# Kernel optimization log

Measured on AMD Instinct MI355X. Metric: run time of the kernel, lower is better.

The kernel has to match this reference:

```python
import jax, jax.numpy as jnp
import numpy as np

TEMPERATURE = 0.1  # init arg `temperature`


def _l2_normalize(x):
    return x / jnp.sqrt(jnp.sum(x * x, axis=1, keepdims=True))


def setup_inputs() -> dict:
    key = jax.random.key(0)
    k1, k2, k3 = jax.random.split(key, 3)
    B, D, Q = 2048, 128, 65536
    projections_1 = jax.random.normal(k1, (B, D), dtype=jnp.float32)
    projections_2 = jax.random.normal(k2, (B, D), dtype=jnp.float32)
    # queue is initialized row-l2-normalized in the original module
    feature_queue = _l2_normalize(jax.random.normal(k3, (Q, D), dtype=jnp.float32))
    return {"projections_1": projections_1, "projections_2": projections_2,
            "feature_queue": feature_queue}


def reference(projections_1, projections_2, feature_queue):
    # NNCLR.contrastive_loss (per-sample losses), including nearest_neighbour.
    p1 = _l2_normalize(projections_1)  # [B, D]
    p2 = _l2_normalize(projections_2)  # [B, D]

    def nearest_neighbour(p):
        # [B, Q] similarity -> top-1 index -> gather from queue
        sims = jnp.einsum('bd,qd->bq', p, feature_queue)
        idx = jnp.argmax(sims, axis=1)  # [B]
        nn = feature_queue[idx]         # [B, D]
        # straight-through: value = nn, gradient flows to p
        return p + jax.lax.stop_gradient(nn - p)

    nn1 = nearest_neighbour(p1)
    nn2 = nearest_neighbour(p2)

    s_1_2_1 = jnp.einsum('id,jd->ij', nn1, p2) / TEMPERATURE
    s_1_2_2 = jnp.einsum('id,jd->ij', p2, nn1) / TEMPERATURE
    s_2_1_1 = jnp.einsum('id,jd->ij', nn2, p1) / TEMPERATURE
    s_2_1_2 = jnp.einsum('id,jd->ij', p1, nn2) / TEMPERATURE

    logits = jnp.concatenate([s_1_2_1, s_1_2_2, s_2_1_1, s_2_1_2], axis=0)  # [4B, B]
    B = p1.shape[0]
    labels = jnp.tile(jnp.arange(B), 4)  # [4B]
    logp = jax.nn.log_softmax(logits, axis=1)
    loss = -jnp.take_along_axis(logp, labels[:, None], axis=1)[:, 0]  # [4B]
    return loss
```

## Files before the change

### kernel.cpp

```cpp
#include <hip/hip_runtime.h>

#define S 132
#define SCALE 10.0f
#define EPS_MARGIN 0.008f
#define SROWS_CAP 480
#define ROWCHUNK 48
#define STRIP_CAND 256

typedef __attribute__((ext_vector_type(8))) short short8;
typedef __attribute__((ext_vector_type(4))) float floatx4;

#define MFMA16(a, b, c) __builtin_amdgcn_mfma_f32_16x16x32_bf16((a), (b), (c), 0, 0, 0)

__device__ __forceinline__ unsigned int ordered_bits(float f) {
    unsigned int b = __float_as_uint(f);
    return (b & 0x80000000u) ? ~b : (b | 0x80000000u);
}
__device__ __forceinline__ float from_ordered(unsigned int u) {
    return __uint_as_float((u & 0x80000000u) ? (u ^ 0x80000000u) : ~u);
}
__device__ __forceinline__ short bf_rne(float x) {
    unsigned int u = __float_as_uint(x);
    return (short)((u + 0x7FFFu + ((u >> 16) & 1u)) >> 16);
}
__device__ __forceinline__ float bf2f(short s) {
    return __uint_as_float(((unsigned int)(unsigned short)s) << 16);
}

__global__ void k_prep(const float* __restrict__ p1, const float* __restrict__ p2,
                       float* __restrict__ pn, short* __restrict__ pnb,
                       unsigned int* __restrict__ mbest,
                       unsigned long long* __restrict__ best,
                       unsigned int* __restrict__ scnt,
                       float* __restrict__ sums) {
    int row = blockIdx.x;
    int t = threadIdx.x;
    const float* src = (row < 2048) ? (p1 + (size_t)row * 128)
                                    : (p2 + (size_t)(row - 2048) * 128);
    float2 v = ((const float2*)src)[t];
    float ss = v.x * v.x + v.y * v.y;
    #pragma unroll
    for (int o = 32; o; o >>= 1) ss += __shfl_xor(ss, o);
    float inv = 1.0f / sqrtf(ss);
    float2 o2; o2.x = v.x * inv; o2.y = v.y * inv;
    ((float2*)(pn + (size_t)row * 128))[t] = o2;
    unsigned int pk = (unsigned int)(unsigned short)bf_rne(o2.x)
                    | ((unsigned int)(unsigned short)bf_rne(o2.y) << 16);
    ((unsigned int*)(pnb + (size_t)row * 128))[t] = pk;
    if (t == 0) { mbest[row] = 0u; best[row] = 0ULL; if (row < 1024) scnt[row] = 0u; }
    if (row < 128) sums[row * 64 + t] = 0.0f;
}

__global__ void k_qcvt(const float* __restrict__ queue, short* __restrict__ qb) {
    size_t i = ((size_t)blockIdx.x * 256 + threadIdx.x) * 8;
    float4 f0 = *(const float4*)(queue + i);
    float4 f1 = *(const float4*)(queue + i + 4);
    short8 o;
    o[0] = bf_rne(f0.x); o[1] = bf_rne(f0.y); o[2] = bf_rne(f0.z); o[3] = bf_rne(f0.w);
    o[4] = bf_rne(f1.x); o[5] = bf_rne(f1.y); o[6] = bf_rne(f1.z); o[7] = bf_rne(f1.w);
    *(short8*)(qb + i) = o;
}

__device__ __forceinline__ void screen_tile(const short8 A[8][4],
                                            short8 b0, short8 b1, short8 b2, short8 b3,
                                            float rmax[8][4]) {
    floatx4 acc[8];
    floatx4 zero = {0.0f, 0.0f, 0.0f, 0.0f};
    #pragma unroll
    for (int rf = 0; rf < 8; ++rf) acc[rf] = MFMA16(A[rf][0], b0, zero);
    #pragma unroll
    for (int rf = 0; rf < 8; ++rf) acc[rf] = MFMA16(A[rf][1], b1, acc[rf]);
    #pragma unroll
    for (int rf = 0; rf < 8; ++rf) acc[rf] = MFMA16(A[rf][2], b2, acc[rf]);
    #pragma unroll
    for (int rf = 0; rf < 8; ++rf) acc[rf] = MFMA16(A[rf][3], b3, acc[rf]);
    #pragma unroll
    for (int rf = 0; rf < 8; ++rf)
        #pragma unroll
        for (int r = 0; r < 4; ++r) rmax[rf][r] = fmaxf(rmax[rf][r], acc[rf][r]);
}

__global__ __launch_bounds__(256, 2) void k_screen(const short* __restrict__ pnb,
                                                   const short* __restrict__ qb,
                                                   unsigned int* __restrict__ mbest,
                                                   float* __restrict__ smax) {
    int tid = threadIdx.x;
    int lane = tid & 63, wv = tid >> 6;
    int n16 = lane & 15, quad = lane >> 4;

    int id = blockIdx.x;
    int xcd = id & 7;
    int g = id >> 3;
    int rowblk = g & 7;
    int qsub = g >> 3;
    int qsplit = xcd * 8 + qsub;
    int rowbase = rowblk * 512 + wv * 128;
    int qstart = qsplit * 1024;

    short8 A[8][4];
    #pragma unroll
    for (int rf = 0; rf < 8; ++rf) {
        const short* ap = pnb + (size_t)(rowbase + rf * 16 + n16) * 128 + quad * 8;
        #pragma unroll
        for (int kk = 0; kk < 4; ++kk)
            A[rf][kk] = *(const short8*)(ap + kk * 32);
    }
    #pragma unroll
    for (int rf = 0; rf < 8; ++rf)
        #pragma unroll
        for (int kk = 0; kk < 4; ++kk)
            asm volatile("" : "+v"(A[rf][kk]));

    float rmax[8][4];
    #pragma unroll
    for (int rf = 0; rf < 8; ++rf)
        #pragma unroll
        for (int r = 0; r < 4; ++r) rmax[rf][r] = -1e30f;

    const short* lp = qb + (size_t)(qstart + n16) * 128 + quad * 8;
    short8 a0 = *(const short8*)(lp), a1 = *(const short8*)(lp + 32),
           a2 = *(const short8*)(lp + 64), a3 = *(const short8*)(lp + 96);

    for (int t = 0; t < 64; t += 2) {
        if ((t & 15) == 0) __syncthreads();
        const short* p1p = lp + 2048;
        short8 b0 = *(const short8*)(p1p), b1 = *(const short8*)(p1p + 32),
               b2 = *(const short8*)(p1p + 64), b3 = *(const short8*)(p1p + 96);
        screen_tile(A, a0, a1, a2, a3, rmax);
        const short* p2p = lp + 4096;
        a0 = *(const short8*)(p2p); a1 = *(const short8*)(p2p + 32);
        a2 = *(const short8*)(p2p + 64); a3 = *(const short8*)(p2p + 96);
        screen_tile(A, b0, b1, b2, b3, rmax);
        lp += 4096;
    }

    #pragma unroll
    for (int rf = 0; rf < 8; ++rf)
        #pragma unroll
        for (int r = 0; r < 4; ++r) {
            float v = rmax[rf][r];
            v = fmaxf(v, __shfl_xor(v, 1));
            v = fmaxf(v, __shfl_xor(v, 2));
            v = fmaxf(v, __shfl_xor(v, 4));
            v = fmaxf(v, __shfl_xor(v, 8));
            if (n16 == 0) {
                int row = rowbase + rf * 16 + quad * 4 + r;
                atomicMax(&mbest[row], ordered_bits(v));
                smax[(size_t)qsplit * 4096 + row] = v;
            }
        }
}

__global__ __launch_bounds__(256) void k_rows(const unsigned int* __restrict__ mbest,
                                              const float* __restrict__ smax,
                                              int* __restrict__ rcnt,
                                              unsigned short* __restrict__ rlist) {
    __shared__ unsigned short rows[SROWS_CAP];
    __shared__ int nsh;
    int tid = threadIdx.x;
    int s = blockIdx.x;
    if (tid == 0) nsh = 0;
    __syncthreads();
    const float* sm = smax + (size_t)s * 4096;
    #pragma unroll
    for (int j = 0; j < 16; ++j) {
        int row = tid + 256 * j;
        float thr = from_ordered(mbest[row]) - EPS_MARGIN;
        if (sm[row] > thr) {
            int pos = atomicAdd(&nsh, 1);
            if (pos < SROWS_CAP) rows[pos] = (unsigned short)row;
        }
    }
    __syncthreads();
    int n = nsh; if (n > SROWS_CAP) n = SROWS_CAP;
    if (tid == 0) rcnt[s] = n;
    for (int i = tid; i < n; i += 256) rlist[s * SROWS_CAP + i] = rows[i];
}

__global__ __launch_bounds__(256, 4) void k_rescreen(const short* __restrict__ pnb,
                                                     const short* __restrict__ qb,
                                                     const unsigned int* __restrict__ mbest,
                                                     const int* __restrict__ rcnt,
                                                     const unsigned short* __restrict__ rlist,
                                                     unsigned int* __restrict__ scnt,
                                                     unsigned int* __restrict__ cand) {
    int b = blockIdx.x;
    int s = b & 63;
    int qp = b >> 6;
    int n = rcnt[s];
    if (n == 0) return;

    int tid = threadIdx.x;
    int lane = tid & 63, wv = tid >> 6;
    int n16 = lane & 15, quad = lane >> 4;
    int qt = qp * 4 + wv;
    int qrow = s * 1024 + qt * 16 + n16;

    const short* bp = qb + (size_t)qrow * 128 + quad * 8;
    short8 b0 = *(const short8*)(bp);
    short8 b1 = *(const short8*)(bp + 32);
    short8 b2 = *(const short8*)(bp + 64);
    short8 b3 = *(const short8*)(bp + 96);

    const unsigned short* rl = rlist + s * SROWS_CAP;
    for (int base = 0; base < n; base += ROWCHUNK) {
        short8 Af[3][4]; float th[3][4]; int rowC[3][4];
        #pragma unroll
        for (int rt = 0; rt < 3; ++rt) {
            int ia = base + rt * 16 + n16;
            int rA = rl[ia < n ? ia : base];
            const short* ap = pnb + (size_t)rA * 128 + quad * 8;
            #pragma unroll
            for (int kk = 0; kk < 4; ++kk) Af[rt][kk] = *(const short8*)(ap + kk * 32);
            #pragma unroll
            for (int r = 0; r < 4; ++r) {
                int ic = base + rt * 16 + quad * 4 + r;
                if (ic < n) {
                    int rr = rl[ic];
                    rowC[rt][r] = rr;
                    th[rt][r] = from_ordered(mbest[rr]) - EPS_MARGIN;
                } else { rowC[rt][r] = 0; th[rt][r] = 3.0e38f; }
            }
        }
        #pragma unroll
        for (int rt = 0; rt < 3; ++rt) {
            floatx4 zero = {0.0f, 0.0f, 0.0f, 0.0f};
            floatx4 acc = MFMA16(Af[rt][0], b0, zero);
            acc = MFMA16(Af[rt][1], b1, acc);
            acc = MFMA16(Af[rt][2], b2, acc);
            acc = MFMA16(Af[rt][3], b3, acc);
            #pragma unroll
            for (int r = 0; r < 4; ++r) {
                if (acc[r] > th[rt][r]) {
                    unsigned int pos = atomicAdd(&scnt[s * 16], 1u);
                    if (pos < STRIP_CAND)
                        cand[s * STRIP_CAND + pos] =
                            ((unsigned int)rowC[rt][r] << 16) | (unsigned int)(qrow & 0xFFFF);
                }
            }
        }
    }
}

__global__ void k_rerank(const float* __restrict__ pn, const float* __restrict__ queue,
                         const unsigned int* __restrict__ scnt,
                         const unsigned int* __restrict__ cand,
                         unsigned long long* __restrict__ best) {
    int lane = threadIdx.x & 63, wv = threadIdx.x >> 6;
    int s = blockIdx.x >> 2;
    int wq = ((blockIdx.x & 3) << 2) | wv;
    unsigned int c = scnt[s * 16]; if (c > STRIP_CAND) c = STRIP_CAND;
    for (unsigned int slot = wq; slot < c; slot += 16) {
        unsigned int v = cand[s * STRIP_CAND + slot];
        unsigned int row = v >> 16;
        unsigned int q = v & 0xFFFFu;
        float2 a = ((const float2*)(pn + (size_t)row * 128))[lane];
        float2 b = ((const float2*)(queue + (size_t)q * 128))[lane];
        float d = a.x * b.x + a.y * b.y;
        #pragma unroll
        for (int o = 32; o; o >>= 1) d += __shfl_xor(d, o);
        if (lane == 0) {
            unsigned long long pk = ((unsigned long long)ordered_bits(d) << 32)
                                  | (unsigned long long)(unsigned int)(~q);
            atomicMax(&best[row], pk);
        }
    }
}

__global__ void k_gather(const float* __restrict__ queue,
                         const unsigned long long* __restrict__ best,
                         short* __restrict__ nnb) {
    int row = blockIdx.x;
    int t = threadIdx.x;
    unsigned int idx = ~(unsigned int)(best[row] & 0xFFFFFFFFull);
    idx &= 0xFFFFu;
    float2 v = ((const float2*)(queue + (size_t)idx * 128))[t];
    unsigned int pk = (unsigned int)(unsigned short)bf_rne(v.x)
                    | ((unsigned int)(unsigned short)bf_rne(v.y) << 16);
    ((unsigned int*)(nnb + (size_t)row * 128))[t] = pk;
}

__global__ __launch_bounds__(256) void k_gemm_lse(const short* __restrict__ Ab,
                                                  const float* __restrict__ B,
                                                  float* __restrict__ rowsum,
                                                  float* __restrict__ colsum,
                                                  float* __restrict__ diag) {
    __shared__ __align__(16) float al[64 * S];
    __shared__ __align__(16) float bl[64 * S];
    __shared__ float red[64][17];
    int tid = threadIdx.x;
    const short8* asrc = (const short8*)(Ab + (size_t)blockIdx.x * 64 * 128);
    #pragma unroll
    for (int i = tid; i < 1024; i += 256) {
        short8 v = asrc[i];
        int r = i >> 4, c = (i & 15) * 8;
        float* dst = &al[r * S + c];
        #pragma unroll
        for (int j = 0; j < 8; ++j) dst[j] = bf2f(v[j]);
    }
    const float4* bsrc = (const float4*)(B + (size_t)blockIdx.y * 64 * 128);
    #pragma unroll
    for (int i = tid; i < 2048; i += 256) {
        int r = i >> 5, c = i & 31;
        *(float4*)&bl[r * S + c * 4] = bsrc[i];
    }
    __syncthreads();
    int ty = tid >> 4, tx = tid & 15;
    float acc[4][4] = {};
    #pragma unroll 2
    for (int k = 0; k < 128; k += 4) {
        float4 a[4], b[4];
        #pragma unroll
        for (int i = 0; i < 4; ++i) a[i] = *(const float4*)&al[(ty + 16 * i) * S + k];
        #pragma unroll
        for (int j = 0; j < 4; ++j) b[j] = *(const float4*)&bl[(tx + 16 * j) * S + k];
        #pragma unroll
        for (int i = 0; i < 4; ++i)
            #pragma unroll
            for (int j = 0; j < 4; ++j)
                acc[i][j] += a[i].x * b[j].x + a[i].y * b[j].y +
                             a[i].z * b[j].z + a[i].w * b[j].w;
    }
    int rowbase = blockIdx.x * 64, colbase = blockIdx.y * 64;

    float e[4][4], rs[4], cs[4];
    #pragma unroll
    for (int i = 0; i < 4; ++i) { rs[i] = 0.0f; cs[i] = 0.0f; }
    #pragma unroll
    for (int i = 0; i < 4; ++i)
        #pragma unroll
        for (int j = 0; j < 4; ++j) {
            e[i][j] = __expf(acc[i][j] * SCALE - 10.0f);
            rs[i] += e[i][j];
        }
    #pragma unroll
    for (int j = 0; j < 4; ++j)
        #pragma unroll
        for (int i = 0; i < 4; ++i) cs[j] += e[i][j];

    if (rowbase == colbase && ty == tx) {
        #pragma unroll
        for (int i = 0; i < 4; ++i) diag[rowbase + ty + 16 * i] = acc[i][i];
    }

    #pragma unroll
    for (int i = 0; i < 4; ++i) red[ty + 16 * i][tx] = rs[i];
    __syncthreads();
    if (tid < 64) {
        float s = 0.0f;
        #pragma unroll
        for (int x = 0; x < 16; ++x) s += red[tid][x];
        atomicAdd(&rowsum[rowbase + tid], s);
    }
    __syncthreads();
    #pragma unroll
    for (int j = 0; j < 4; ++j) red[tx + 16 * j][ty] = cs[j];
    __syncthreads();
    if (tid < 64) {
        float s = 0.0f;
        #pragma unroll
        for (int x = 0; x < 16; ++x) s += red[tid][x];
        atomicAdd(&colsum[colbase + tid], s);
    }
}

__global__ void k_final(const float* __restrict__ sums,
                        const float* __restrict__ dg1, const float* __restrict__ dg2,
                        float* __restrict__ out) {
    int idx = blockIdx.x * 256 + threadIdx.x;
    int seg = idx >> 11, r = idx & 2047;
    float s = sums[seg * 2048 + r];
    float d = (seg < 2) ? dg1[r] : dg2[r];
    out[idx] = 10.0f + logf(s) - d * SCALE;
}

extern "C" void kernel_launch(void* const* d_in, const int* in_sizes, int n_in,
                              void* d_out, int out_size, void* d_ws, size_t ws_size,
                              hipStream_t stream) {
    const float* p1    = (const float*)d_in[0];
    const float* p2    = (const float*)d_in[1];
    const float* queue = (const float*)d_in[2];
    float* out = (float*)d_out;

    char* w = (char*)d_ws;
    float* pn  = (float*)w;
    short* nnb = (short*)(w + (2u << 20));
    short* qb  = (short*)(w + (3u << 20));
    short* pnb = (short*)(w + (19u << 20));
    char* b2 = w + (20u << 20);
    unsigned int* mbest = (unsigned int*)b2;
    unsigned long long* best = (unsigned long long*)(b2 + (16u << 10));
    unsigned int* scnt = (unsigned int*)(b2 + (48u << 10));
    int* rcnt = (int*)(b2 + (52u << 10));
    unsigned short* rlist = (unsigned short*)(b2 + (56u << 10));
    unsigned int* cand = (unsigned int*)(b2 + (116u << 10));
    float* sums = (float*)(b2 + (180u << 10));
    float* dg1  = sums + 8192;
    float* dg2  = dg1 + 2048;
    float* smax = (float*)nnb;

    k_prep<<<4096, 64, 0, stream>>>(p1, p2, pn, pnb, mbest, best, scnt, sums);
    k_qcvt<<<4096, 256, 0, stream>>>(queue, qb);
    k_screen<<<512, 256, 0, stream>>>(pnb, qb, mbest, smax);
    k_rows<<<64, 256, 0, stream>>>(mbest, smax, rcnt, rlist);
    k_rescreen<<<64 * 16, 256, 0, stream>>>(pnb, qb, mbest, rcnt, rlist, scnt, cand);
    k_rerank<<<256, 256, 0, stream>>>(pn, queue, scnt, cand, best);
    k_gather<<<4096, 64, 0, stream>>>(queue, best, nnb);

    k_gemm_lse<<<dim3(32, 32), 256, 0, stream>>>(nnb, pn + 2048 * 128,
                                                 sums, sums + 2048, dg1);
    k_gemm_lse<<<dim3(32, 32), 256, 0, stream>>>(nnb + 2048 * 128, pn,
                                                 sums + 4096, sums + 6144, dg2);
    k_final<<<32, 256, 0, stream>>>(sums, dg1, dg2, out);
}
```

Baseline: 252.8 us.

## Fuse pipeline kernels: merge prep/qcvt, inline row selection and rerank, gather into GEMM

Combines the normalization and queue bf16 conversion into one launch. Rebuilds the per-strip candidate row list inside each rescreen block instead of in a separate kernel, and does the exact fp32 rerank in-wave via ballot instead of writing a candidate buffer. The nearest-neighbour gather is folded into the GEMM tile load, and the two GEMM launches become one 3D grid. This drops several launches and intermediate buffers. In exchange, the row-list scan is repeated by 16 blocks per strip, and the rerank now runs serially inside the screening waves.

```diff
diff --git a/kernel.cpp b/kernel.cpp
--- a/kernel.cpp
+++ b/kernel.cpp
@@ -5,7 +5,6 @@
 #define EPS_MARGIN 0.008f
 #define SROWS_CAP 480
 #define ROWCHUNK 48
-#define STRIP_CAND 256
 
 typedef __attribute__((ext_vector_type(8))) short short8;
 typedef __attribute__((ext_vector_type(4))) float floatx4;
@@ -27,38 +26,43 @@
     return __uint_as_float(((unsigned int)(unsigned short)s) << 16);
 }
 
-__global__ void k_prep(const float* __restrict__ p1, const float* __restrict__ p2,
-                       float* __restrict__ pn, short* __restrict__ pnb,
-                       unsigned int* __restrict__ mbest,
-                       unsigned long long* __restrict__ best,
-                       unsigned int* __restrict__ scnt,
-                       float* __restrict__ sums) {
-    int row = blockIdx.x;
-    int t = threadIdx.x;
-    const float* src = (row < 2048) ? (p1 + (size_t)row * 128)
-                                    : (p2 + (size_t)(row - 2048) * 128);
-    float2 v = ((const float2*)src)[t];
-    float ss = v.x * v.x + v.y * v.y;
-    #pragma unroll
-    for (int o = 32; o; o >>= 1) ss += __shfl_xor(ss, o);
-    float inv = 1.0f / sqrtf(ss);
-    float2 o2; o2.x = v.x * inv; o2.y = v.y * inv;
-    ((float2*)(pn + (size_t)row * 128))[t] = o2;
-    unsigned int pk = (unsigned int)(unsigned short)bf_rne(o2.x)
-                    | ((unsigned int)(unsigned short)bf_rne(o2.y) << 16);
-    ((unsigned int*)(pnb + (size_t)row * 128))[t] = pk;
-    if (t == 0) { mbest[row] = 0u; best[row] = 0ULL; if (row < 1024) scnt[row] = 0u; }
-    if (row < 128) sums[row * 64 + t] = 0.0f;
-}
-
-__global__ void k_qcvt(const float* __restrict__ queue, short* __restrict__ qb) {
-    size_t i = ((size_t)blockIdx.x * 256 + threadIdx.x) * 8;
-    float4 f0 = *(const float4*)(queue + i);
-    float4 f1 = *(const float4*)(queue + i + 4);
-    short8 o;
-    o[0] = bf_rne(f0.x); o[1] = bf_rne(f0.y); o[2] = bf_rne(f0.z); o[3] = bf_rne(f0.w);
-    o[4] = bf_rne(f1.x); o[5] = bf_rne(f1.y); o[6] = bf_rne(f1.z); o[7] = bf_rne(f1.w);
-    *(short8*)(qb + i) = o;
+__global__ __launch_bounds__(256) void k_prep_qcvt(const float* __restrict__ p1,
+                                                   const float* __restrict__ p2,
+                                                   const float* __restrict__ queue,
+                                                   float* __restrict__ pn,
+                                                   short* __restrict__ pnb,
+                                                   short* __restrict__ qb,
+                                                   unsigned int* __restrict__ mbest,
+                                                   unsigned long long* __restrict__ best,
+                                                   float* __restrict__ sums) {
+    int b = blockIdx.x;
+    if (b < 1024) {
+        int sub = threadIdx.x >> 6;
+        int t = threadIdx.x & 63;
+        int row = b * 4 + sub;
+        const float* src = (row < 2048) ? (p1 + (size_t)row * 128)
+                                        : (p2 + (size_t)(row - 2048) * 128);
+        float2 v = ((const float2*)src)[t];
+        float ss = v.x * v.x + v.y * v.y;
+        #pragma unroll
+        for (int o = 32; o; o >>= 1) ss += __shfl_xor(ss, o);
+        float inv = 1.0f / sqrtf(ss);
+        float2 o2; o2.x = v.x * inv; o2.y = v.y * inv;
+        ((float2*)(pn + (size_t)row * 128))[t] = o2;
+        unsigned int pk = (unsigned int)(unsigned short)bf_rne(o2.x)
+                        | ((unsigned int)(unsigned short)bf_rne(o2.y) << 16);
+        ((unsigned int*)(pnb + (size_t)row * 128))[t] = pk;
+        if (t == 0) { mbest[row] = 0u; best[row] = 0ULL; }
+        if (row < 128) sums[row * 64 + t] = 0.0f;
+    } else {
+        size_t i = ((size_t)(b - 1024) * 256 + threadIdx.x) * 8;
+        float4 f0 = *(const float4*)(queue + i);
+        float4 f1 = *(const float4*)(queue + i + 4);
+        short8 o;
+        o[0] = bf_rne(f0.x); o[1] = bf_rne(f0.y); o[2] = bf_rne(f0.z); o[3] = bf_rne(f0.w);
+        o[4] = bf_rne(f1.x); o[5] = bf_rne(f1.y); o[6] = bf_rne(f1.z); o[7] = bf_rne(f1.w);
+        *(short8*)(qb + i) = o;
+    }
 }
 
 __device__ __forceinline__ void screen_tile(const short8 A[8][4],
@@ -151,14 +155,19 @@
         }
 }
 
-__global__ __launch_bounds__(256) void k_rows(const unsigned int* __restrict__ mbest,
-                                              const float* __restrict__ smax,
-                                              int* __restrict__ rcnt,
-                                              unsigned short* __restrict__ rlist) {
+__global__ __launch_bounds__(256, 4) void k_rescreen(const short* __restrict__ pnb,
+                                                     const short* __restrict__ qb,
+                                                     const unsigned int* __restrict__ mbest,
+                                                     const float* __restrict__ smax,
+                                                     const float* __restrict__ pn,
+                                                     const float* __restrict__ queue,
+                                                     unsigned long long* __restrict__ best) {
     __shared__ unsigned short rows[SROWS_CAP];
     __shared__ int nsh;
+    int b = blockIdx.x;
+    int s = b & 63;
+    int qp = b >> 6;
     int tid = threadIdx.x;
-    int s = blockIdx.x;
     if (tid == 0) nsh = 0;
     __syncthreads();
     const float* sm = smax + (size_t)s * 4096;
@@ -173,24 +182,8 @@
     }
     __syncthreads();
     int n = nsh; if (n > SROWS_CAP) n = SROWS_CAP;
-    if (tid == 0) rcnt[s] = n;
-    for (int i = tid; i < n; i += 256) rlist[s * SROWS_CAP + i] = rows[i];
-}
-
-__global__ __launch_bounds__(256, 4) void k_rescreen(const short* __restrict__ pnb,
-                                                     const short* __restrict__ qb,
-                                                     const unsigned int* __restrict__ mbest,
-                                                     const int* __restrict__ rcnt,
-                                                     const unsigned short* __restrict__ rlist,
-                                                     unsigned int* __restrict__ scnt,
-                                                     unsigned int* __restrict__ cand) {
-    int b = blockIdx.x;
-    int s = b & 63;
-    int qp = b >> 6;
-    int n = rcnt[s];
     if (n == 0) return;
 
-    int tid = threadIdx.x;
     int lane = tid & 63, wv = tid >> 6;
     int n16 = lane & 15, quad = lane >> 4;
     int qt = qp * 4 + wv;
@@ -202,13 +195,12 @@
     short8 b2 = *(const short8*)(bp + 64);
     short8 b3 = *(const short8*)(bp + 96);
 
-    const unsigned short* rl = rlist + s * SROWS_CAP;
     for (int base = 0; base < n; base += ROWCHUNK) {
         short8 Af[3][4]; float th[3][4]; int rowC[3][4];
         #pragma unroll
         for (int rt = 0; rt < 3; ++rt) {
             int ia = base + rt * 16 + n16;
-            int rA = rl[ia < n ? ia : base];
+            int rA = rows[ia < n ? ia : base];
             const short* ap = pnb + (size_t)rA * 128 + quad * 8;
             #pragma unroll
             for (int kk = 0; kk < 4; ++kk) Af[rt][kk] = *(const short8*)(ap + kk * 32);
@@ -216,7 +208,7 @@
             for (int r = 0; r < 4; ++r) {
                 int ic = base + rt * 16 + quad * 4 + r;
                 if (ic < n) {
-                    int rr = rl[ic];
+                    int rr = rows[ic];
                     rowC[rt][r] = rr;
                     th[rt][r] = from_ordered(mbest[rr]) - EPS_MARGIN;
                 } else { rowC[rt][r] = 0; th[rt][r] = 3.0e38f; }
@@ -231,72 +223,56 @@
             acc = MFMA16(Af[rt][3], b3, acc);
             #pragma unroll
             for (int r = 0; r < 4; ++r) {
-                if (acc[r] > th[rt][r]) {
-                    unsigned int pos = atomicAdd(&scnt[s * 16], 1u);
-                    if (pos < STRIP_CAND)
-                        cand[s * STRIP_CAND + pos] =
-                            ((unsigned int)rowC[rt][r] << 16) | (unsigned int)(qrow & 0xFFFF);
+                unsigned long long mb = __ballot(acc[r] > th[rt][r]);
+                while (mb) {
+                    int L = __builtin_ctzll(mb);
+                    mb &= mb - 1;
+                    int row = __shfl(rowC[rt][r], L);
+                    int q   = __shfl(qrow, L);
+                    float2 a  = ((const float2*)(pn + (size_t)row * 128))[lane];
+                    float2 bq = ((const float2*)(queue + (size_t)q * 128))[lane];
+                    float d = a.x * bq.x + a.y * bq.y;
+                    #pragma unroll
+                    for (int o = 32; o; o >>= 1) d += __shfl_xor(d, o);
+                    if (lane == 0) {
+                        unsigned long long pk = ((unsigned long long)ordered_bits(d) << 32)
+                                              | (unsigned long long)(unsigned int)(~q);
+                        atomicMax(&best[row], pk);
+                    }
                 }
             }
         }
     }
 }
 
-__global__ void k_rerank(const float* __restrict__ pn, const float* __restrict__ queue,
-                         const unsigned int* __restrict__ scnt,
-                         const unsigned int* __restrict__ cand,
-                         unsigned long long* __restrict__ best) {
-    int lane = threadIdx.x & 63, wv = threadIdx.x >> 6;
-    int s = blockIdx.x >> 2;
-    int wq = ((blockIdx.x & 3) << 2) | wv;
-    unsigned int c = scnt[s * 16]; if (c > STRIP_CAND) c = STRIP_CAND;
-    for (unsigned int slot = wq; slot < c; slot += 16) {
-        unsigned int v = cand[s * STRIP_CAND + slot];
-        unsigned int row = v >> 16;
-        unsigned int q = v & 0xFFFFu;
-        float2 a = ((const float2*)(pn + (size_t)row * 128))[lane];
-        float2 b = ((const float2*)(queue + (size_t)q * 128))[lane];
-        float d = a.x * b.x + a.y * b.y;
-        #pragma unroll
-        for (int o = 32; o; o >>= 1) d += __shfl_xor(d, o);
-        if (lane == 0) {
-            unsigned long long pk = ((unsigned long long)ordered_bits(d) << 32)
-                                  | (unsigned long long)(unsigned int)(~q);
-            atomicMax(&best[row], pk);
-        }
-    }
-}
-
-__global__ void k_gather(const float* __restrict__ queue,
-                         const unsigned long long* __restrict__ best,
-                         short* __restrict__ nnb) {
-    int row = blockIdx.x;
-    int t = threadIdx.x;
-    unsigned int idx = ~(unsigned int)(best[row] & 0xFFFFFFFFull);
-    idx &= 0xFFFFu;
-    float2 v = ((const float2*)(queue + (size_t)idx * 128))[t];
-    unsigned int pk = (unsigned int)(unsigned short)bf_rne(v.x)
-                    | ((unsigned int)(unsigned short)bf_rne(v.y) << 16);
-    ((unsigned int*)(nnb + (size_t)row * 128))[t] = pk;
-}
-
-__global__ __launch_bounds__(256) void k_gemm_lse(const short* __restrict__ Ab,
-                                                  const float* __restrict__ B,
-                                                  float* __restrict__ rowsum,
-                                                  float* __restrict__ colsum,
-                                                  float* __restrict__ diag) {
+__global__ __launch_bounds__(256) void k_gemm_lse(const unsigned long long* __restrict__ best,
+                                                  const float* __restrict__ queue,
+                                                  const float* __restrict__ pn,
+                                                  float* __restrict__ sums,
+                                                  float* __restrict__ dg) {
     __shared__ __align__(16) float al[64 * S];
     __shared__ __align__(16) float bl[64 * S];
     __shared__ float red[64][17];
     int tid = threadIdx.x;
-    const short8* asrc = (const short8*)(Ab + (size_t)blockIdx.x * 64 * 128);
+    int z = blockIdx.z;
+    const float* B = pn + (z ? 0 : 2048 * 128);
+    float* rowsum = sums + z * 4096;
+    float* colsum = sums + z * 4096 + 2048;
+    float* diag = dg + z * 2048;
+    int arow0 = z * 2048 + blockIdx.x * 64;
+
     #pragma unroll
     for (int i = tid; i < 1024; i += 256) {
-        short8 v = asrc[i];
         int r = i >> 4, c = (i & 15) * 8;
+        unsigned int idx = (~(unsigned int)(best[arow0 + r] & 0xFFFFFFFFull)) & 0xFFFFu;
+        const float* qr = queue + (size_t)idx * 128 + c;
+        float4 f0 = *(const float4*)(qr);
+        float4 f1 = *(const float4*)(qr + 4);
         float* dst = &al[r * S + c];
-        #pragma unroll
-        for (int j = 0; j < 8; ++j) dst[j] = bf2f(v[j]);
+        dst[0] = bf2f(bf_rne(f0.x)); dst[1] = bf2f(bf_rne(f0.y));
+        dst[2] = bf2f(bf_rne(f0.z)); dst[3] = bf2f(bf_rne(f0.w));
+        dst[4] = bf2f(bf_rne(f1.x)); dst[5] = bf2f(bf_rne(f1.y));
+        dst[6] = bf2f(bf_rne(f1.z)); dst[7] = bf2f(bf_rne(f1.w));
     }
     const float4* bsrc = (const float4*)(B + (size_t)blockIdx.y * 64 * 128);
     #pragma unroll
@@ -383,33 +359,20 @@
     float* out = (float*)d_out;
 
     char* w = (char*)d_ws;
-    float* pn  = (float*)w;
-    short* nnb = (short*)(w + (2u << 20));
-    short* qb  = (short*)(w + (3u << 20));
-    short* pnb = (short*)(w + (19u << 20));
+    float* pn   = (float*)w;
+    float* smax = (float*)(w + (2u << 20));
+    short* qb   = (short*)(w + (3u << 20));
+    short* pnb  = (short*)(w + (19u << 20));
     char* b2 = w + (20u << 20);
     unsigned int* mbest = (unsigned int*)b2;
     unsigned long long* best = (unsigned long long*)(b2 + (16u << 10));
-    unsigned int* scnt = (unsigned int*)(b2 + (48u << 10));
-    int* rcnt = (int*)(b2 + (52u << 10));
-    unsigned short* rlist = (unsigned short*)(b2 + (56u << 10));
-    unsigned int* cand = (unsigned int*)(b2 + (116u << 10));
-    float* sums = (float*)(b2 + (180u << 10));
+    float* sums = (float*)(b2 + (48u << 10));
     float* dg1  = sums + 8192;
     float* dg2  = dg1 + 2048;
-    float* smax = (float*)nnb;
-
-    k_prep<<<4096, 64, 0, stream>>>(p1, p2, pn, pnb, mbest, best, scnt, sums);
-    k_qcvt<<<4096, 256, 0, stream>>>(queue, qb);
+
+    k_prep_qcvt<<<5120, 256, 0, stream>>>(p1, p2, queue, pn, pnb, qb, mbest, best, sums);
     k_screen<<<512, 256, 0, stream>>>(pnb, qb, mbest, smax);
-    k_rows<<<64, 256, 0, stream>>>(mbest, smax, rcnt, rlist);
-    k_rescreen<<<64 * 16, 256, 0, stream>>>(pnb, qb, mbest, rcnt, rlist, scnt, cand);
-    k_rerank<<<256, 256, 0, stream>>>(pn, queue, scnt, cand, best);
-    k_gather<<<4096, 64, 0, stream>>>(queue, best, nnb);
-
-    k_gemm_lse<<<dim3(32, 32), 256, 0, stream>>>(nnb, pn + 2048 * 128,
-                                                 sums, sums + 2048, dg1);
-    k_gemm_lse<<<dim3(32, 32), 256, 0, stream>>>(nnb + 2048 * 128, pn,
-                                                 sums + 4096, sums + 6144, dg2);
+    k_rescreen<<<64 * 16, 256, 0, stream>>>(pnb, qb, mbest, smax, pn, queue, best);
+    k_gemm_lse<<<dim3(32, 32, 2), 256, 0, stream>>>(best, queue, pn, sums, dg1);
     k_final<<<32, 256, 0, stream>>>(sums, dg1, dg2, out);
 }
```

Result: faster. 234.8 us (-7.1%).
